# Kernel tuning notes

Hardware: AMD Instinct MI355X
Metric: run time of the kernel (lower is better)

Reference implementation:

```python
import jax, jax.numpy as jnp
import numpy as np

SCENARIO_DIM = 10
ACTION_DIM = 2
N_EXPERTS = 8
EXP_H = 32
GATE_H = 64
B = 1048576


def setup_inputs() -> dict:
    key = jax.random.key(0)
    ks = jax.random.split(key, 16)
    s = 0.1
    return {
        "x": jax.random.normal(ks[0], (B, SCENARIO_DIM), dtype=jnp.float32),
        # stacked expert MLP params: Linear(10->32), Linear(32->32), Linear(32->2)
        "W1": jax.random.normal(ks[1], (N_EXPERTS, SCENARIO_DIM, EXP_H), dtype=jnp.float32) * s,
        "b1": jax.random.normal(ks[2], (N_EXPERTS, EXP_H), dtype=jnp.float32) * s,
        "W2": jax.random.normal(ks[3], (N_EXPERTS, EXP_H, EXP_H), dtype=jnp.float32) * s,
        "b2": jax.random.normal(ks[4], (N_EXPERTS, EXP_H), dtype=jnp.float32) * s,
        "W3": jax.random.normal(ks[5], (N_EXPERTS, EXP_H, ACTION_DIM), dtype=jnp.float32) * s,
        "b3": jax.random.normal(ks[6], (N_EXPERTS, ACTION_DIM), dtype=jnp.float32) * s,
        # gating: Linear(10->64), Linear(64->n_experts)
        "G1": jax.random.normal(ks[7], (SCENARIO_DIM, GATE_H), dtype=jnp.float32) * s,
        "gb1": jax.random.normal(ks[8], (GATE_H,), dtype=jnp.float32) * s,
        "G2": jax.random.normal(ks[9], (GATE_H, N_EXPERTS), dtype=jnp.float32) * s,
        "gb2": jax.random.normal(ks[10], (N_EXPERTS,), dtype=jnp.float32) * s,
        # refine: Linear(2+10->64), Linear(64->2)
        "R1": jax.random.normal(ks[11], (ACTION_DIM + SCENARIO_DIM, GATE_H), dtype=jnp.float32) * s,
        "rb1": jax.random.normal(ks[12], (GATE_H,), dtype=jnp.float32) * s,
        "R2": jax.random.normal(ks[13], (GATE_H, ACTION_DIM), dtype=jnp.float32) * s,
        "rb2": jax.random.normal(ks[14], (ACTION_DIM,), dtype=jnp.float32) * s,
    }


def reference(x, W1, b1, W2, b2, W3, b3, G1, gb1, G2, gb2, R1, rb1, R2, rb2):
    # batched expert MLPs: (B, E, H)
    h = jax.nn.relu(jnp.einsum("bd,edh->beh", x, W1) + b1)
    h = jax.nn.relu(jnp.einsum("beh,ehk->bek", h, W2) + b2)
    outs = jnp.tanh(jnp.einsum("beh,eha->bea", h, W3) + b3)  # (B, E, A)
    # gating softmax over experts
    g = jax.nn.relu(x @ G1 + gb1)
    w = jax.nn.softmax(g @ G2 + gb2, axis=-1)  # (B, E)
    fused = jnp.einsum("bea,be->ba", outs, w)  # (B, A)
    # refine head
    r = jax.nn.relu(jnp.concatenate([fused, x], axis=-1) @ R1 + rb1)
    return jnp.tanh(r @ R2 + rb2)
```

## Files before the change

### kernel.cpp

```cpp
#include <hip/hip_runtime.h>


#define B_TOTAL 1048576
#define NFRAG   60
#define FRAG_U4 (NFRAG * 64)

typedef _Float16 f16x8 __attribute__((ext_vector_type(8)));
typedef __fp16   fp16x2 __attribute__((ext_vector_type(2)));
typedef float    f32x16 __attribute__((ext_vector_type(16)));
typedef unsigned int u32x4v __attribute__((ext_vector_type(4)));

#define MFMA(a, b, c) __builtin_amdgcn_mfma_f32_32x32x16_f16((a), (b), (c), 0, 0, 0)

__device__ __forceinline__ unsigned pkrtz_u(float a, float b) {
    fp16x2 t = __builtin_amdgcn_cvt_pkrtz(a, b);
    return __builtin_bit_cast(unsigned, t);
}
__device__ __forceinline__ unsigned pkru(float a, float b) {
    fp16x2 t = __builtin_amdgcn_cvt_pkrtz(a, b);
    fp16x2 z = {(__fp16)0.f, (__fp16)0.f};
    fp16x2 m = __builtin_elementwise_max(t, z);
    return __builtin_bit_cast(unsigned, m);
}
__device__ __forceinline__ f16x8 mk4(unsigned a, unsigned b, unsigned c, unsigned d) {
    u32x4v t; t.x = a; t.y = b; t.z = c; t.w = d;
    return __builtin_bit_cast(f16x8, t);
}
__device__ __forceinline__ void packrelu(const f32x16& c, unsigned* p) {
    #pragma unroll
    for (int i = 0; i < 8; ++i)
        p[i] = pkru(c[2 * i], c[2 * i + 1]);
}
__device__ __forceinline__ float tanh_fast(float v) {
    v = fminf(fmaxf(v, -10.f), 10.f);
    float e = __expf(2.f * v);
    return __fdividef(e - 1.f, e + 1.f);
}

__global__ void prep_kernel(const float* __restrict__ W1, const float* __restrict__ b1,
                            const float* __restrict__ W2, const float* __restrict__ b2,
                            const float* __restrict__ W3, const float* __restrict__ b3,
                            const float* __restrict__ G1, const float* __restrict__ gb1,
                            const float* __restrict__ G2, const float* __restrict__ gb2,
                            const float* __restrict__ R1, const float* __restrict__ rb1,
                            const float* __restrict__ R2, const float* __restrict__ rb2,
                            _Float16* __restrict__ ws)
{
    int gid = blockIdx.x * 256 + threadIdx.x;
    if (gid >= NFRAG * 64) return;
    int f = gid >> 6, lane = gid & 63;
    int m = lane & 31, h = lane >> 5;
    float v[8];
    #pragma unroll
    for (int j = 0; j < 8; ++j) v[j] = 0.f;

    if (f < 2) {
        int mo = f * 32 + m;
        for (int j = 0; j < 8; ++j) {
            if (h == 0)       v[j] = G1[j * 64 + mo];
            else if (j < 2)   v[j] = G1[(8 + j) * 64 + mo];
            else if (j == 2)  v[j] = gb1[mo];
        }
    } else if (f < 6) {
        int s = f - 2;
        for (int j = 0; j < 8; ++j) {
            int k = 32 * (s >> 1) + 16 * (s & 1) + (j & 3) + 8 * (j >> 2) + 4 * h;
            v[j] = (m < 8) ? G2[k * 8 + m] : 0.f;
        }
    } else if (f < 8) {
        int mo = (f - 6) * 32 + m;
        for (int j = 0; j < 8; ++j) {
            if (h == 0)       v[j] = R1[j * 64 + mo];
            else if (j < 4)   v[j] = R1[(8 + j) * 64 + mo];
            else if (j == 4)  v[j] = rb1[mo];
        }
    } else if (f < 12) {
        int s = f - 8;
        for (int j = 0; j < 8; ++j) {
            int k = 32 * (s >> 1) + 16 * (s & 1) + (j & 3) + 8 * (j >> 2) + 4 * h;
            v[j] = (m < 2) ? R2[k * 2 + m] : 0.f;
        }
    } else {
        int e = (f - 12) / 6, t = (f - 12) % 6;
        if (t == 0) {
            for (int j = 0; j < 8; ++j) {
                if (h == 0)       v[j] = W1[e * 320 + j * 32 + m];
                else if (j < 2)   v[j] = W1[e * 320 + (8 + j) * 32 + m];
                else if (j == 2)  v[j] = b1[e * 32 + m];
            }
        } else if (t == 1 || t == 2) {
            int s = t - 1;
            for (int j = 0; j < 8; ++j) {
                int k = 16 * s + (j & 3) + 8 * (j >> 2) + 4 * h;
                v[j] = W2[e * 1024 + k * 32 + m];
            }
        } else if (t == 3) {
            if (h == 0) v[0] = b2[e * 32 + m];
        } else {
            int s = t - 4;
            for (int j = 0; j < 8; ++j) {
                int k = 16 * s + (j & 3) + 8 * (j >> 2) + 4 * h;
                v[j] = (m < 2) ? W3[e * 64 + k * 2 + m] : 0.f;
            }
        }
    }
    _Float16* dst = ws + (size_t)(f * 64 + lane) * 8;
    #pragma unroll
    for (int j = 0; j < 8; ++j) dst[j] = (_Float16)v[j];
}

__global__ __launch_bounds__(1024, 2) void brain_mfma(
    const float* __restrict__ x,
    const u32x4v* __restrict__ wsf,
    const float* __restrict__ b3, const float* __restrict__ gb2,
    const float* __restrict__ rb2,
    float* __restrict__ out)
{
    __shared__ u32x4v smem[FRAG_U4];
    const int tid = threadIdx.x;
    for (int i = tid; i < FRAG_U4; i += 1024) smem[i] = wsf[i];
    __syncthreads();

    const int lane = tid & 63;
    const int wv   = tid >> 6;
    const int n    = lane & 31;
    const int h    = lane >> 5;
    const size_t sA = (size_t)blockIdx.x * 1024 + wv * 64 + n;
    const size_t sB = sA + 32;

    const unsigned ONEZERO = 0x00003C00u;

    const float2* xpA = (const float2*)(x + sA * 10);
    const float2* xpB = (const float2*)(x + sB * 10);
    float2 A0 = xpA[h ? 3 : 0], A1 = xpA[h ? 4 : 1], A2 = xpA[h ? 4 : 2], A3 = xpA[3];
    float2 B0 = xpB[h ? 3 : 0], B1 = xpB[h ? 4 : 1], B2 = xpB[h ? 4 : 2], B3 = xpB[3];

    unsigned pkAa = pkrtz_u(A0.x, A0.y), pkAb = pkrtz_u(A1.x, A1.y);
    unsigned pkAc = pkrtz_u(A2.x, A2.y), pkAd = pkrtz_u(A3.x, A3.y);
    unsigned pkBa = pkrtz_u(B0.x, B0.y), pkBb = pkrtz_u(B1.x, B1.y);
    unsigned pkBc = pkrtz_u(B2.x, B2.y), pkBd = pkrtz_u(B3.x, B3.y);

    f16x8 xfA = h ? mk4(pkAb, ONEZERO, 0u, 0u) : mk4(pkAa, pkAb, pkAc, pkAd);
    f16x8 xfB = h ? mk4(pkBb, ONEZERO, 0u, 0u) : mk4(pkBa, pkBb, pkBc, pkBd);

    const f16x8 ONES = mk4(0x3C003C00u, 0x3C003C00u, 0x3C003C00u, 0x3C003C00u);
    f32x16 Z;
    #pragma unroll
    for (int i = 0; i < 16; ++i) Z[i] = 0.f;

    #define FRAG(F) __builtin_bit_cast(f16x8, smem[(F) * 64 + lane])

    float wA[8], wB[8];
    {
        f16x8 g0 = FRAG(0), g1 = FRAG(1);
        f32x16 cg0A = MFMA(g0, xfA, Z), cg1A = MFMA(g1, xfA, Z);
        f32x16 cg0B = MFMA(g0, xfB, Z), cg1B = MFMA(g1, xfB, Z);
        unsigned p0A[8], p1A[8], p0B[8], p1B[8];
        packrelu(cg0A, p0A); packrelu(cg1A, p1A);
        packrelu(cg0B, p0B); packrelu(cg1B, p1B);
        f16x8 l0 = FRAG(2), l1 = FRAG(3), l2 = FRAG(4), l3 = FRAG(5);
        f32x16 clA = MFMA(l0, mk4(p0A[0], p0A[1], p0A[2], p0A[3]), Z);
        clA = MFMA(l1, mk4(p0A[4], p0A[5], p0A[6], p0A[7]), clA);
        clA = MFMA(l2, mk4(p1A[0], p1A[1], p1A[2], p1A[3]), clA);
        clA = MFMA(l3, mk4(p1A[4], p1A[5], p1A[6], p1A[7]), clA);
        f32x16 clB = MFMA(l0, mk4(p0B[0], p0B[1], p0B[2], p0B[3]), Z);
        clB = MFMA(l1, mk4(p0B[4], p0B[5], p0B[6], p0B[7]), clB);
        clB = MFMA(l2, mk4(p1B[0], p1B[1], p1B[2], p1B[3]), clB);
        clB = MFMA(l3, mk4(p1B[4], p1B[5], p1B[6], p1B[7]), clB);

        float lA[8], lB[8];
        #pragma unroll
        for (int j = 0; j < 4; ++j) {
            lA[j]     = clA[j] + gb2[j];
            lA[4 + j] = __shfl_xor(clA[j], 32) + gb2[4 + j];
            lB[j]     = clB[j] + gb2[j];
            lB[4 + j] = __shfl_xor(clB[j], 32) + gb2[4 + j];
        }
        float mxA = lA[0], mxB = lB[0];
        #pragma unroll
        for (int j = 1; j < 8; ++j) { mxA = fmaxf(mxA, lA[j]); mxB = fmaxf(mxB, lB[j]); }
        float sA_ = 0.f, sB_ = 0.f;
        #pragma unroll
        for (int j = 0; j < 8; ++j) {
            wA[j] = __expf(lA[j] - mxA); sA_ += wA[j];
            wB[j] = __expf(lB[j] - mxB); sB_ += wB[j];
        }
        float invA = __fdividef(1.f, sA_), invB = __fdividef(1.f, sB_);
        #pragma unroll
        for (int j = 0; j < 8; ++j) { wA[j] *= invA; wB[j] *= invB; }
    }

    float fA0 = 0.f, fA1 = 0.f, fB0 = 0.f, fB1 = 0.f;
    #pragma unroll 1
    for (int e = 0; e < 8; ++e) {
        const int fb = 12 + e * 6;
        f16x8 a0 = FRAG(fb);
        f32x16 c1A = MFMA(a0, xfA, Z);
        f32x16 c1B = MFMA(a0, xfB, Z);
        unsigned qA[8], qB[8];
        packrelu(c1A, qA); packrelu(c1B, qB);

        f16x8 a1 = FRAG(fb + 1), a2 = FRAG(fb + 2), a3 = FRAG(fb + 3);
        f32x16 c2A = MFMA(a1, mk4(qA[0], qA[1], qA[2], qA[3]), Z);
        c2A = MFMA(a2, mk4(qA[4], qA[5], qA[6], qA[7]), c2A);
        c2A = MFMA(a3, ONES, c2A);
        f32x16 c2B = MFMA(a1, mk4(qB[0], qB[1], qB[2], qB[3]), Z);
        c2B = MFMA(a2, mk4(qB[4], qB[5], qB[6], qB[7]), c2B);
        c2B = MFMA(a3, ONES, c2B);
        packrelu(c2A, qA); packrelu(c2B, qB);

        f16x8 a4 = FRAG(fb + 4), a5 = FRAG(fb + 5);
        f32x16 c3A = MFMA(a4, mk4(qA[0], qA[1], qA[2], qA[3]), Z);
        c3A = MFMA(a5, mk4(qA[4], qA[5], qA[6], qA[7]), c3A);
        f32x16 c3B = MFMA(a4, mk4(qB[0], qB[1], qB[2], qB[3]), Z);
        c3B = MFMA(a5, mk4(qB[4], qB[5], qB[6], qB[7]), c3B);

        float b30 = b3[2 * e], b31 = b3[2 * e + 1];
        fA0 = fmaf(wA[e], tanh_fast(c3A[0] + b30), fA0);
        fA1 = fmaf(wA[e], tanh_fast(c3A[1] + b31), fA1);
        fB0 = fmaf(wB[e], tanh_fast(c3B[0] + b30), fB0);
        fB1 = fmaf(wB[e], tanh_fast(c3B[1] + b31), fB1);
    }

    unsigned rxA0 = h ? pkAa : pkrtz_u(fA0, fA1);
    unsigned rxB0 = h ? pkBa : pkrtz_u(fB0, fB1);
    unsigned rxA1 = h ? pkAb : pkAa, rxA2 = h ? ONEZERO : pkAb, rxA3 = h ? 0u : pkAc;
    unsigned rxB1 = h ? pkBb : pkBa, rxB2 = h ? ONEZERO : pkBb, rxB3 = h ? 0u : pkBc;
    f16x8 rfA = mk4(rxA0, rxA1, rxA2, rxA3);
    f16x8 rfB = mk4(rxB0, rxB1, rxB2, rxB3);

    f16x8 r0 = FRAG(6), r1 = FRAG(7);
    f32x16 cr0A = MFMA(r0, rfA, Z), cr1A = MFMA(r1, rfA, Z);
    f32x16 cr0B = MFMA(r0, rfB, Z), cr1B = MFMA(r1, rfB, Z);
    unsigned p0A[8], p1A[8], p0B[8], p1B[8];
    packrelu(cr0A, p0A); packrelu(cr1A, p1A);
    packrelu(cr0B, p0B); packrelu(cr1B, p1B);

    f16x8 d0 = FRAG(8), d1 = FRAG(9), d2 = FRAG(10), d3 = FRAG(11);
    f32x16 cdA = MFMA(d0, mk4(p0A[0], p0A[1], p0A[2], p0A[3]), Z);
    cdA = MFMA(d1, mk4(p0A[4], p0A[5], p0A[6], p0A[7]), cdA);
    cdA = MFMA(d2, mk4(p1A[0], p1A[1], p1A[2], p1A[3]), cdA);
    cdA = MFMA(d3, mk4(p1A[4], p1A[5], p1A[6], p1A[7]), cdA);
    f32x16 cdB = MFMA(d0, mk4(p0B[0], p0B[1], p0B[2], p0B[3]), Z);
    cdB = MFMA(d1, mk4(p0B[4], p0B[5], p0B[6], p0B[7]), cdB);
    cdB = MFMA(d2, mk4(p1B[0], p1B[1], p1B[2], p1B[3]), cdB);
    cdB = MFMA(d3, mk4(p1B[4], p1B[5], p1B[6], p1B[7]), cdB);

    if (h == 0) {
        float2 oA, oB;
        oA.x = tanh_fast(cdA[0] + rb2[0]);
        oA.y = tanh_fast(cdA[1] + rb2[1]);
        oB.x = tanh_fast(cdB[0] + rb2[0]);
        oB.y = tanh_fast(cdB[1] + rb2[1]);
        ((float2*)out)[sA] = oA;
        ((float2*)out)[sB] = oB;
    }
}

extern "C" void kernel_launch(void* const* d_in, const int* in_sizes, int n_in,
                              void* d_out, int out_size, void* d_ws, size_t ws_size,
                              hipStream_t stream) {
    const float* x   = (const float*)d_in[0];
    const float* W1  = (const float*)d_in[1];
    const float* b1  = (const float*)d_in[2];
    const float* W2  = (const float*)d_in[3];
    const float* b2  = (const float*)d_in[4];
    const float* W3  = (const float*)d_in[5];
    const float* b3  = (const float*)d_in[6];
    const float* G1  = (const float*)d_in[7];
    const float* gb1 = (const float*)d_in[8];
    const float* G2  = (const float*)d_in[9];
    const float* gb2 = (const float*)d_in[10];
    const float* R1  = (const float*)d_in[11];
    const float* rb1 = (const float*)d_in[12];
    const float* R2  = (const float*)d_in[13];
    const float* rb2 = (const float*)d_in[14];
    float* out = (float*)d_out;
    _Float16* ws = (_Float16*)d_ws;

    hipLaunchKernelGGL(prep_kernel, dim3(15), dim3(256), 0, stream,
                       W1, b1, W2, b2, W3, b3, G1, gb1, G2, gb2, R1, rb1, R2, rb2, ws);
    hipLaunchKernelGGL(brain_mfma, dim3(B_TOTAL / 1024), dim3(1024), 0, stream,
                       x, (const u32x4v*)ws, b3, gb2, rb2, out);
}
```

Before: 161.9 us.

## Fuse weight-fragment prep into main kernel and pin MFMA accumulators

Removes the separate prep kernel launch. Each block now builds the fp16 MFMA weight fragments straight from the raw fp32 parameters into shared memory. This saves a launch and the workspace round trip, but every one of the 1024 blocks repeats the scattered fragment construction. Empty asm constraints are also added to pin accumulator vectors in VGPRs, to stop the compiler from rematerializing or reordering them.

```diff
diff --git a/kernel.cpp b/kernel.cpp
--- a/kernel.cpp
+++ b/kernel.cpp
@@ -11,6 +11,7 @@
 typedef unsigned int u32x4v __attribute__((ext_vector_type(4)));
 
 #define MFMA(a, b, c) __builtin_amdgcn_mfma_f32_32x32x16_f16((a), (b), (c), 0, 0, 0)
+#define PIN(X) asm("" : "+v"(X))
 
 __device__ __forceinline__ unsigned pkrtz_u(float a, float b) {
     fp16x2 t = __builtin_amdgcn_cvt_pkrtz(a, b);
@@ -37,20 +38,17 @@
     return __fdividef(e - 1.f, e + 1.f);
 }
 
-__global__ void prep_kernel(const float* __restrict__ W1, const float* __restrict__ b1,
+__device__ void frag_values(int f, int lane,
+                            const float* __restrict__ W1, const float* __restrict__ b1,
                             const float* __restrict__ W2, const float* __restrict__ b2,
-                            const float* __restrict__ W3, const float* __restrict__ b3,
+                            const float* __restrict__ W3,
                             const float* __restrict__ G1, const float* __restrict__ gb1,
-                            const float* __restrict__ G2, const float* __restrict__ gb2,
+                            const float* __restrict__ G2,
                             const float* __restrict__ R1, const float* __restrict__ rb1,
-                            const float* __restrict__ R2, const float* __restrict__ rb2,
-                            _Float16* __restrict__ ws)
+                            const float* __restrict__ R2,
+                            float v[8])
 {
-    int gid = blockIdx.x * 256 + threadIdx.x;
-    if (gid >= NFRAG * 64) return;
-    int f = gid >> 6, lane = gid & 63;
     int m = lane & 31, h = lane >> 5;
-    float v[8];
     #pragma unroll
     for (int j = 0; j < 8; ++j) v[j] = 0.f;
 
@@ -104,21 +102,31 @@
             }
         }
     }
-    _Float16* dst = ws + (size_t)(f * 64 + lane) * 8;
-    #pragma unroll
-    for (int j = 0; j < 8; ++j) dst[j] = (_Float16)v[j];
 }
 
 __global__ __launch_bounds__(1024, 2) void brain_mfma(
     const float* __restrict__ x,
-    const u32x4v* __restrict__ wsf,
-    const float* __restrict__ b3, const float* __restrict__ gb2,
-    const float* __restrict__ rb2,
+    const float* __restrict__ W1, const float* __restrict__ b1,
+    const float* __restrict__ W2, const float* __restrict__ b2,
+    const float* __restrict__ W3, const float* __restrict__ b3,
+    const float* __restrict__ G1, const float* __restrict__ gb1,
+    const float* __restrict__ G2, const float* __restrict__ gb2,
+    const float* __restrict__ R1, const float* __restrict__ rb1,
+    const float* __restrict__ R2, const float* __restrict__ rb2,
     float* __restrict__ out)
 {
     __shared__ u32x4v smem[FRAG_U4];
     const int tid = threadIdx.x;
-    for (int i = tid; i < FRAG_U4; i += 1024) smem[i] = wsf[i];
+
+    for (int idx = tid; idx < FRAG_U4; idx += 1024) {
+        int f = idx >> 6, ln = idx & 63;
+        float v[8];
+        frag_values(f, ln, W1, b1, W2, b2, W3, G1, gb1, G2, R1, rb1, R2, v);
+        f16x8 hv;
+        #pragma unroll
+        for (int j = 0; j < 8; ++j) hv[j] = (_Float16)v[j];
+        smem[idx] = __builtin_bit_cast(u32x4v, hv);
+    }
     __syncthreads();
 
     const int lane = tid & 63;
@@ -147,6 +155,7 @@
     f32x16 Z;
     #pragma unroll
     for (int i = 0; i < 16; ++i) Z[i] = 0.f;
+    PIN(Z);
 
     #define FRAG(F) __builtin_bit_cast(f16x8, smem[(F) * 64 + lane])
 
@@ -155,6 +164,7 @@
         f16x8 g0 = FRAG(0), g1 = FRAG(1);
         f32x16 cg0A = MFMA(g0, xfA, Z), cg1A = MFMA(g1, xfA, Z);
         f32x16 cg0B = MFMA(g0, xfB, Z), cg1B = MFMA(g1, xfB, Z);
+        PIN(cg0A); PIN(cg1A); PIN(cg0B); PIN(cg1B);
         unsigned p0A[8], p1A[8], p0B[8], p1B[8];
         packrelu(cg0A, p0A); packrelu(cg1A, p1A);
         packrelu(cg0B, p0B); packrelu(cg1B, p1B);
@@ -167,6 +177,7 @@
         clB = MFMA(l1, mk4(p0B[4], p0B[5], p0B[6], p0B[7]), clB);
         clB = MFMA(l2, mk4(p1B[0], p1B[1], p1B[2], p1B[3]), clB);
         clB = MFMA(l3, mk4(p1B[4], p1B[5], p1B[6], p1B[7]), clB);
+        PIN(clA); PIN(clB);
 
         float lA[8], lB[8];
         #pragma unroll
@@ -197,6 +208,7 @@
         f16x8 a0 = FRAG(fb);
         f32x16 c1A = MFMA(a0, xfA, Z);
         f32x16 c1B = MFMA(a0, xfB, Z);
+        PIN(c1A); PIN(c1B);
         unsigned qA[8], qB[8];
         packrelu(c1A, qA); packrelu(c1B, qB);
 
@@ -207,6 +219,7 @@
         f32x16 c2B = MFMA(a1, mk4(qB[0], qB[1], qB[2], qB[3]), Z);
         c2B = MFMA(a2, mk4(qB[4], qB[5], qB[6], qB[7]), c2B);
         c2B = MFMA(a3, ONES, c2B);
+        PIN(c2A); PIN(c2B);
         packrelu(c2A, qA); packrelu(c2B, qB);
 
         f16x8 a4 = FRAG(fb + 4), a5 = FRAG(fb + 5);
@@ -214,6 +227,7 @@
         c3A = MFMA(a5, mk4(qA[4], qA[5], qA[6], qA[7]), c3A);
         f32x16 c3B = MFMA(a4, mk4(qB[0], qB[1], qB[2], qB[3]), Z);
         c3B = MFMA(a5, mk4(qB[4], qB[5], qB[6], qB[7]), c3B);
+        PIN(c3A); PIN(c3B);
 
         float b30 = b3[2 * e], b31 = b3[2 * e + 1];
         fA0 = fmaf(wA[e], tanh_fast(c3A[0] + b30), fA0);
@@ -232,6 +246,7 @@
     f16x8 r0 = FRAG(6), r1 = FRAG(7);
     f32x16 cr0A = MFMA(r0, rfA, Z), cr1A = MFMA(r1, rfA, Z);
     f32x16 cr0B = MFMA(r0, rfB, Z), cr1B = MFMA(r1, rfB, Z);
+    PIN(cr0A); PIN(cr1A); PIN(cr0B); PIN(cr1B);
     unsigned p0A[8], p1A[8], p0B[8], p1B[8];
     packrelu(cr0A, p0A); packrelu(cr1A, p1A);
     packrelu(cr0B, p0B); packrelu(cr1B, p1B);
@@ -245,6 +260,7 @@
     cdB = MFMA(d1, mk4(p0B[4], p0B[5], p0B[6], p0B[7]), cdB);
     cdB = MFMA(d2, mk4(p1B[0], p1B[1], p1B[2], p1B[3]), cdB);
     cdB = MFMA(d3, mk4(p1B[4], p1B[5], p1B[6], p1B[7]), cdB);
+    PIN(cdA); PIN(cdB);
 
     if (h == 0) {
         float2 oA, oB;
@@ -276,10 +292,8 @@
     const float* R2  = (const float*)d_in[13];
     const float* rb2 = (const float*)d_in[14];
     float* out = (float*)d_out;
-    _Float16* ws = (_Float16*)d_ws;
-
-    hipLaunchKernelGGL(prep_kernel, dim3(15), dim3(256), 0, stream,
-                       W1, b1, W2, b2, W3, b3, G1, gb1, G2, gb2, R1, rb1, R2, rb2, ws);
+
     hipLaunchKernelGGL(brain_mfma, dim3(B_TOTAL / 1024), dim3(1024), 0, stream,
-                       x, (const u32x4v*)ws, b3, gb2, rb2, out);
-}
+                       x, W1, b1, W2, b2, W3, b3, G1, gb1, G2, gb2,
+                       R1, rb1, R2, rb2, out);
+}
```

After: 170.0 us. 5.0% more time.
